# Performance work log

Hardware: AMD Instinct MI355X
Metric: run time of the kernel (lower is better)

Reference implementation:

```python
import jax, jax.numpy as jnp
import numpy as np

B, S, D = 4, 2048, 512
H = 8
DK = D // H
F = 2048  # filter_size
K = 9     # kernel_size
PAD = (K - 1) // 2
EPS = 1e-5


def layer_norm(x, gamma, beta):
    mu = jnp.mean(x, axis=-1, keepdims=True)
    var = jnp.var(x, axis=-1, keepdims=True)
    return (x - mu) * jax.lax.rsqrt(var + EPS) * gamma + beta


def conv1d(x_bcs, w_oik, b):
    # x: (B, C, S), w: (O, I, K) torch Conv1d layout, SAME padding
    y = jax.lax.conv_general_dilated(
        x_bcs, w_oik, window_strides=(1,), padding=[(PAD, PAD)],
        dimension_numbers=("NCH", "OIH", "NCH"))
    return y + b[None, :, None]


def setup_inputs() -> dict:
    key = jax.random.key(0)
    ks = jax.random.split(key, 16)
    g = lambda k, shp: (jax.random.normal(k, shp, dtype=jnp.float32) * 0.02)
    return {
        "src": jax.random.normal(ks[0], (B, S, D), dtype=jnp.float32),
        "src_mask": jnp.ones((B, 1, S), dtype=bool),
        "wq": g(ks[1], (D, D)), "bq": jnp.zeros((D,), jnp.float32),
        "wk": g(ks[2], (D, D)), "bk": jnp.zeros((D,), jnp.float32),
        "wv": g(ks[3], (D, D)), "bv": jnp.zeros((D,), jnp.float32),
        "wo": g(ks[4], (D, D)), "bo": jnp.zeros((D,), jnp.float32),
        "conv1_w": g(ks[5], (F, D, K)), "conv1_b": jnp.zeros((F,), jnp.float32),
        "conv2_w": g(ks[6], (D, F, K)), "conv2_b": jnp.zeros((D,), jnp.float32),
        "g1": jnp.ones((D,), jnp.float32), "b1": jnp.zeros((D,), jnp.float32),
        "g2": jnp.ones((D,), jnp.float32), "b2": jnp.zeros((D,), jnp.float32),
    }


def reference(src, src_mask, wq, bq, wk, bk, wv, bv, wo, bo,
              conv1_w, conv1_b, conv2_w, conv2_b, g1, b1, g2, b2):
    # ---- multi-head self attention (naive, explicit score matrix) ----
    q = (src @ wq.T + bq).reshape(B, S, H, DK).transpose(0, 2, 1, 3)  # (B,H,S,DK)
    k = (src @ wk.T + bk).reshape(B, S, H, DK).transpose(0, 2, 1, 3)
    v = (src @ wv.T + bv).reshape(B, S, H, DK).transpose(0, 2, 1, 3)
    scores = jnp.einsum("bhqd,bhkd->bhqk", q, k) / jnp.sqrt(jnp.float32(DK))
    mask4 = src_mask[:, None, :, :]  # (B,1,1,S) broadcast over heads/queries
    scores = jnp.where(mask4, scores, jnp.float32(-1e9))
    attn = jax.nn.softmax(scores, axis=-1)
    ctx = jnp.einsum("bhqk,bhkd->bhqd", attn, v)
    ctx = ctx.transpose(0, 2, 1, 3).reshape(B, S, D)
    attn_out = ctx @ wo.T + bo
    x = layer_norm(src + attn_out, g1, b1)
    # ---- conv1d FFN ----
    h = x.transpose(0, 2, 1)                       # (B, D, S)
    h = jax.nn.relu(conv1d(h, conv1_w, conv1_b))   # (B, F, S)
    h = conv1d(h, conv2_w, conv2_b)                # (B, D, S)
    ffn_out = h.transpose(0, 2, 1)
    return layer_norm(x + ffn_out, g2, b2)
```

## Files before the change

kernel.cpp:

```cpp
#include <hip/hip_runtime.h>


#define DEV __device__ __forceinline__

typedef __attribute__((ext_vector_type(8))) short bf16x8_t;
typedef __attribute__((ext_vector_type(4))) float f32x4_t;

DEV unsigned short f2bf(float f) {
  union { float f; unsigned u; } c; c.f = f;
  return (unsigned short)((c.u + 0x7fffu + ((c.u >> 16) & 1u)) >> 16);
}
DEV float bf2f(unsigned short h) {
  union { unsigned u; float f; } c; c.u = ((unsigned)h) << 16;
  return c.f;
}

DEV void stage16(const unsigned short* g, unsigned short* lds_base, int lane) {
#if __has_builtin(__builtin_amdgcn_global_load_lds)
  (void)lane;
  __builtin_amdgcn_global_load_lds(
      (const __attribute__((address_space(1))) void*)g,
      (__attribute__((address_space(3))) void*)lds_base, 16, 0, 0);
#else
  *(bf16x8_t*)(lds_base + lane * 8) = *(const bf16x8_t*)g;
#endif
}

template <int CK, int OUTMODE, int N, int K, int LDA, int LDO, int KSPLIT>
__global__ __launch_bounds__(256, 4) void gemm_bt(
    const unsigned short* __restrict__ A, const unsigned short* __restrict__ B,
    const float* __restrict__ bias, void* __restrict__ out, void* __restrict__ out2,
    long pstride) {
  __shared__ __align__(16) unsigned short As[2][128 * 32];
  __shared__ __align__(16) unsigned short Bs[2][128 * 32];
  const int tid = threadIdx.x;
  const int lane = tid & 63, wave = tid >> 6;
  const int quad = lane >> 4, l16 = lane & 15;
  const int bm = blockIdx.x << 7, bn = blockIdx.y << 7;
  const int wr = (wave >> 1) << 6, wc = (wave & 1) << 6;
  const int k0 = blockIdx.z * KSPLIT;

  f32x4_t acc[4][4];
#pragma unroll
  for (int i = 0; i < 4; i++)
#pragma unroll
    for (int j = 0; j < 4; j++) acc[i][j] = (f32x4_t){0.f, 0.f, 0.f, 0.f};

  const int srow = (wave << 4) + (lane >> 2);
  const int scol = (lane & 3) << 3;

#pragma unroll 1
  for (int kb = 0; kb < KSPLIT; kb += 64) {
    __syncthreads();
#pragma unroll
    for (int h = 0; h < 2; h++) {
      const int k = k0 + kb + (h << 5);
      int ktap, kcol;
      if (CK > 0) { ktap = k / CK; kcol = k % CK; } else { ktap = 0; kcol = k; }
#pragma unroll
      for (int i = 0; i < 2; i++) {
        const int r = (i << 6) + srow;
        const int am = bm + r;
        const int arow = (CK > 0) ? (am + ((am >> 11) << 3) + ktap) : am;
        stage16(A + (long)arow * LDA + kcol + scol, &As[h][(i << 11) + (wave << 9)], lane);
        stage16(B + (long)(bn + r) * K + k + scol, &Bs[h][(i << 11) + (wave << 9)], lane);
      }
    }
    __syncthreads();

#pragma unroll
    for (int h = 0; h < 2; h++) {
      bf16x8_t af[4], bfr[4];
#pragma unroll
      for (int t = 0; t < 4; t++)
        af[t] = *(const bf16x8_t*)&As[h][((wr + (t << 4) + l16) << 5) + (quad << 3)];
#pragma unroll
      for (int t = 0; t < 4; t++)
        bfr[t] = *(const bf16x8_t*)&Bs[h][((wc + (t << 4) + l16) << 5) + (quad << 3)];
#pragma unroll
      for (int mt = 0; mt < 4; mt++)
#pragma unroll
        for (int nt = 0; nt < 4; nt++)
          acc[mt][nt] = __builtin_amdgcn_mfma_f32_16x16x32_bf16(af[mt], bfr[nt],
                                                                acc[mt][nt], 0, 0, 0);
    }
  }

  if (OUTMODE == 4) {
    const bool isqk = (blockIdx.y < 8);
#pragma unroll
    for (int mt = 0; mt < 4; mt++)
#pragma unroll
      for (int nt = 0; nt < 4; nt++) {
        const int col = bn + wc + (nt << 4) + l16;
        const float bv = bias[col];
        const int rowb = bm + wr + (mt << 4) + (quad << 2);
        if (isqk) {
#pragma unroll
          for (int r = 0; r < 4; r++)
            ((unsigned short*)out)[(long)(rowb + r) * 1024 + col] =
                f2bf(acc[mt][nt][r] + bv);
        } else {
          ushort4 pk;
          pk.x = f2bf(acc[mt][nt][0] + bv);
          pk.y = f2bf(acc[mt][nt][1] + bv);
          pk.z = f2bf(acc[mt][nt][2] + bv);
          pk.w = f2bf(acc[mt][nt][3] + bv);
          const int vcol = col - 1024;
          const int bb = rowb >> 11, s = rowb & 2047;
          *(ushort4*)((unsigned short*)out2 + ((long)(bb * 512 + vcol) << 11) + s) = pk;
        }
      }
    return;
  }

  unsigned short* po = (unsigned short*)out;
  if (OUTMODE == 3)
    po = (blockIdx.z == 3) ? (unsigned short*)out2
                           : (unsigned short*)out + (long)blockIdx.z * pstride;
  float* fo = (float*)out;
  if (OUTMODE == 1) fo = (blockIdx.z == 0) ? (float*)out : (float*)out2;

#pragma unroll
  for (int mt = 0; mt < 4; mt++)
#pragma unroll
    for (int nt = 0; nt < 4; nt++) {
      const int col = bn + wc + (nt << 4) + l16;
      float bv = 0.f;
      if (OUTMODE == 0 || OUTMODE == 2) bv = bias[col];
      if (OUTMODE == 1) bv = (blockIdx.z == 0) ? bias[col] : 0.f;
#pragma unroll
      for (int r = 0; r < 4; r++) {
        const int row = bm + wr + (mt << 4) + (quad << 2) + r;
        float v = acc[mt][nt][r] + bv;
        if (OUTMODE == 0) {
          ((unsigned short*)out)[(long)row * LDO + col] = f2bf(v);
        } else if (OUTMODE == 1) {
          fo[(long)row * LDO + col] = v;
        } else if (OUTMODE == 2) {
          v = v > 0.f ? v : 0.f;
          const int orow = row + ((row >> 11) << 3) + 4;
          ((unsigned short*)out)[(long)orow * LDO + col] = f2bf(v);
        } else {
          po[(long)row * LDO + col] = f2bf(v);
        }
      }
    }
}

__global__ __launch_bounds__(256) void flash_attn(
    const unsigned short* __restrict__ qk16, const unsigned short* __restrict__ vT,
    unsigned short* __restrict__ ctx16) {
  __shared__ __align__(16) unsigned short Ks[64 * 64];
  __shared__ __align__(16) unsigned short Vt[64 * 64];
  __shared__ __align__(16) unsigned short Ps[4][2][16 * 80];

  const int tid = threadIdx.x;
  const int lane = tid & 63, wave = tid >> 6;
  const int quad = lane >> 4, l16 = lane & 15;
  const int qt = blockIdx.x, bh = blockIdx.y;
  const int b = bh >> 3, h = bh & 7;
  const long rowbase = (long)b << 11;
  const int hoff = h << 6;
  const int qbase = (qt << 7) + (wave << 5);

  bf16x8_t qa[2][2];
#pragma unroll
  for (int hh = 0; hh < 2; hh++) {
    const long qrow = rowbase + qbase + (hh << 4) + l16;
    qa[hh][0] = *(const bf16x8_t*)(qk16 + (qrow << 10) + hoff + (quad << 3));
    qa[hh][1] = *(const bf16x8_t*)(qk16 + (qrow << 10) + hoff + 32 + (quad << 3));
  }
  bf16x8_t ones;
#pragma unroll
  for (int i = 0; i < 8; i++) ones[i] = (short)0x3F80;

  f32x4_t o[2][4];
#pragma unroll
  for (int hh = 0; hh < 2; hh++)
#pragma unroll
    for (int i = 0; i < 4; i++) o[hh][i] = (f32x4_t){0.f, 0.f, 0.f, 0.f};
  f32x4_t l4[2] = {{0.f, 0.f, 0.f, 0.f}, {0.f, 0.f, 0.f, 0.f}};

  const int srow8 = lane >> 3;
  const int scol8 = (lane & 7) << 3;
  const unsigned short* kbase = qk16 + 512;
  const unsigned short* vbase = vT + ((long)(b * 512 + hoff) << 11);

  for (int kt = 0; kt < 2048; kt += 64) {
    __syncthreads();
#pragma unroll
    for (int j = 0; j < 2; j++) {
      const int kr = (wave << 4) + (j << 3);
      stage16(kbase + ((rowbase + kt + kr + srow8) << 10) + hoff + scol8,
              &Ks[kr << 6], lane);
      stage16(vbase + ((long)(kr + srow8) << 11) + kt + scol8, &Vt[kr << 6], lane);
    }
    __syncthreads();

    bf16x8_t kf[4][2];
#pragma unroll
    for (int t = 0; t < 4; t++) {
      kf[t][0] = *(const bf16x8_t*)&Ks[(((t << 4) + l16) << 6) + (quad << 3)];
      kf[t][1] = *(const bf16x8_t*)&Ks[(((t << 4) + l16) << 6) + 32 + (quad << 3)];
    }
#pragma unroll
    for (int hh = 0; hh < 2; hh++) {
      f32x4_t s[4];
#pragma unroll
      for (int t = 0; t < 4; t++) s[t] = (f32x4_t){0.f, 0.f, 0.f, 0.f};
#pragma unroll
      for (int t = 0; t < 4; t++) {
        s[t] = __builtin_amdgcn_mfma_f32_16x16x32_bf16(qa[hh][0], kf[t][0], s[t], 0, 0, 0);
        s[t] = __builtin_amdgcn_mfma_f32_16x16x32_bf16(qa[hh][1], kf[t][1], s[t], 0, 0, 0);
      }
#pragma unroll
      for (int r = 0; r < 4; r++)
#pragma unroll
        for (int t = 0; t < 4; t++) {
          union { float f; unsigned u; } cv;
          cv.f = __expf(s[t][r] * 0.125f);
          Ps[wave][hh][((quad << 2) + r) * 80 + (t << 4) + l16] =
              (unsigned short)(cv.u >> 16);
        }
    }
    bf16x8_t vf[4][2];
#pragma unroll
    for (int t = 0; t < 4; t++) {
      vf[t][0] = *(const bf16x8_t*)&Vt[(((t << 4) + l16) << 6) + (quad << 3)];
      vf[t][1] = *(const bf16x8_t*)&Vt[(((t << 4) + l16) << 6) + 32 + (quad << 3)];
    }
#pragma unroll
    for (int hh = 0; hh < 2; hh++) {
      const bf16x8_t pa0 = *(const bf16x8_t*)&Ps[wave][hh][l16 * 80 + (quad << 3)];
      const bf16x8_t pa1 = *(const bf16x8_t*)&Ps[wave][hh][l16 * 80 + 32 + (quad << 3)];
      l4[hh] = __builtin_amdgcn_mfma_f32_16x16x32_bf16(pa0, ones, l4[hh], 0, 0, 0);
      l4[hh] = __builtin_amdgcn_mfma_f32_16x16x32_bf16(pa1, ones, l4[hh], 0, 0, 0);
#pragma unroll
      for (int dt = 0; dt < 4; dt++) {
        o[hh][dt] = __builtin_amdgcn_mfma_f32_16x16x32_bf16(pa0, vf[dt][0], o[hh][dt], 0, 0, 0);
        o[hh][dt] = __builtin_amdgcn_mfma_f32_16x16x32_bf16(pa1, vf[dt][1], o[hh][dt], 0, 0, 0);
      }
    }
  }

#pragma unroll
  for (int hh = 0; hh < 2; hh++)
#pragma unroll
    for (int r = 0; r < 4; r++) {
      const float inv = 1.f / l4[hh][r];
      const long orow = rowbase + qbase + (hh << 4) + (quad << 2) + r;
#pragma unroll
      for (int dt = 0; dt < 4; dt++)
        ctx16[(orow << 9) + hoff + (dt << 4) + l16] = f2bf(o[hh][dt][r] * inv);
    }
}

__global__ __launch_bounds__(256) void ln_fused(
    const float* __restrict__ xa, const float* __restrict__ xb,
    const float* __restrict__ xc, const float* __restrict__ gamma,
    const float* __restrict__ beta, unsigned short* __restrict__ padout) {
  const int lane = threadIdx.x & 63, wave = threadIdx.x >> 6;
  const long row = ((long)blockIdx.x << 2) + wave;
  const long base = (row << 9) + (lane << 3);
  float s[8];
  {
    const float4 a0 = *(const float4*)(xa + base);
    const float4 a1 = *(const float4*)(xa + base + 4);
    const float4 b0 = *(const float4*)(xb + base);
    const float4 b1 = *(const float4*)(xb + base + 4);
    const float4 c0 = *(const float4*)(xc + base);
    const float4 c1 = *(const float4*)(xc + base + 4);
    s[0] = a0.x + b0.x + c0.x; s[1] = a0.y + b0.y + c0.y;
    s[2] = a0.z + b0.z + c0.z; s[3] = a0.w + b0.w + c0.w;
    s[4] = a1.x + b1.x + c1.x; s[5] = a1.y + b1.y + c1.y;
    s[6] = a1.z + b1.z + c1.z; s[7] = a1.w + b1.w + c1.w;
  }
  float sum = 0.f, sq = 0.f;
#pragma unroll
  for (int i = 0; i < 8; i++) { sum += s[i]; sq += s[i] * s[i]; }
#pragma unroll
  for (int d = 1; d < 64; d <<= 1) { sum += __shfl_xor(sum, d); sq += __shfl_xor(sq, d); }
  const float mean = sum * (1.f / 512.f);
  const float var = sq * (1.f / 512.f) - mean * mean;
  const float rstd = rsqrtf(var + 1e-5f);
  const int col = lane << 3;
  const long prow = row + ((row >> 11) << 3) + 4;
  bf16x8_t pv;
#pragma unroll
  for (int i = 0; i < 8; i++)
    pv[i] = (short)f2bf((s[i] - mean) * rstd * gamma[col + i] + beta[col + i]);
  *(bf16x8_t*)(padout + (prow << 9) + (lane << 3)) = pv;
}

__global__ __launch_bounds__(256) void ln2_red(
    const unsigned short* __restrict__ xpad, const unsigned short* __restrict__ pA,
    const unsigned short* __restrict__ pB, const float* __restrict__ bias,
    const float* __restrict__ gamma, const float* __restrict__ beta,
    float* __restrict__ out) {
  const int lane = threadIdx.x & 63, wave = threadIdx.x >> 6;
  const long row = ((long)blockIdx.x << 2) + wave;
  const long base = (row << 9) + (lane << 3);
  const int col = lane << 3;
  const long prow = row + ((row >> 11) << 3) + 4;
  const bf16x8_t xr = *(const bf16x8_t*)(xpad + (prow << 9) + (lane << 3));
  const bf16x8_t p0 = *(const bf16x8_t*)(pA + base);
  const bf16x8_t p1 = *(const bf16x8_t*)(pA + 4194304 + base);
  const bf16x8_t p2 = *(const bf16x8_t*)(pA + 8388608 + base);
  const bf16x8_t p3 = *(const bf16x8_t*)(pB + base);
  float s[8];
#pragma unroll
  for (int i = 0; i < 8; i++) {
    s[i] = bf2f((unsigned short)xr[i]) + bias[col + i] +
           bf2f((unsigned short)p0[i]) + bf2f((unsigned short)p1[i]) +
           bf2f((unsigned short)p2[i]) + bf2f((unsigned short)p3[i]);
  }
  float sum = 0.f, sq = 0.f;
#pragma unroll
  for (int i = 0; i < 8; i++) { sum += s[i]; sq += s[i] * s[i]; }
#pragma unroll
  for (int d = 1; d < 64; d <<= 1) { sum += __shfl_xor(sum, d); sq += __shfl_xor(sq, d); }
  const float mean = sum * (1.f / 512.f);
  const float var = sq * (1.f / 512.f) - mean * mean;
  const float rstd = rsqrtf(var + 1e-5f);
  float y[8];
#pragma unroll
  for (int i = 0; i < 8; i++) y[i] = (s[i] - mean) * rstd * gamma[col + i] + beta[col + i];
  float4 y0 = {y[0], y[1], y[2], y[3]}, y1 = {y[4], y[5], y[6], y[7]};
  *(float4*)(out + base) = y0;
  *(float4*)(out + base + 4) = y1;
}

__global__ void prep(const float* __restrict__ src, unsigned short* __restrict__ src16,
                     const float* __restrict__ wq, const float* __restrict__ wk,
                     const float* __restrict__ wv, const float* __restrict__ wo,
                     unsigned short* __restrict__ wqkv16, unsigned short* __restrict__ wo16,
                     const float* __restrict__ c1w, unsigned short* __restrict__ w1p,
                     const float* __restrict__ c2w, unsigned short* __restrict__ w2p,
                     unsigned short* __restrict__ xpad,
                     const float* __restrict__ bq, const float* __restrict__ bk,
                     const float* __restrict__ bv, float* __restrict__ bqkv) {
  const int bid = blockIdx.x, tid = threadIdx.x;
  if (bid < 4096) {
    const int i = bid * 256 + tid;
    const float4 v = ((const float4*)src)[i];
    ushort4 r; r.x = f2bf(v.x); r.y = f2bf(v.y); r.z = f2bf(v.z); r.w = f2bf(v.w);
    ((ushort4*)src16)[i] = r;
  } else if (bid < 5120) {
    const int w = (bid - 4096) >> 8;
    const int i = ((bid - 4096) & 255) * 256 + tid;
    const float* sp = (w == 0) ? wq : (w == 1) ? wk : (w == 2) ? wv : wo;
    unsigned short* dp = (w < 3) ? (wqkv16 + (w << 18)) : wo16;
    const float4 v = ((const float4*)sp)[i];
    ushort4 r; r.x = f2bf(v.x); r.y = f2bf(v.y); r.z = f2bf(v.z); r.w = f2bf(v.w);
    ((ushort4*)dp)[i] = r;
  } else if (bid < 9216) {
    const int idx = (bid - 5120) * 256 + tid;
    const int c = idx & 511, f = idx >> 9;
    float vals[9];
#pragma unroll
    for (int k = 0; k < 9; k++) vals[k] = c1w[(long)idx * 9 + k];
#pragma unroll
    for (int k = 0; k < 9; k++)
      w1p[(((long)f * 9 + k) << 9) + c] = f2bf(vals[k]);
  } else if (bid < 13312) {
    const int idx = (bid - 9216) * 256 + tid;
    const int c = idx & 2047, f = idx >> 11;
    float vals[9];
#pragma unroll
    for (int k = 0; k < 9; k++) vals[k] = c2w[(long)idx * 9 + k];
#pragma unroll
    for (int k = 0; k < 9; k++)
      w2p[(((long)f * 9 + k) << 11) + c] = f2bf(vals[k]);
  } else if (bid < 13376) {
    const int i = (bid - 13312) * 256 + tid;
    const int b = i >> 12, r = (i >> 9) & 7, c = i & 511;
    const int t = (r < 4) ? r : 2048 + r;
    xpad[((long)b * 2056 + t) * 512 + c] = 0;
  } else {
    const int i = (bid - 13376) * 256 + tid;
    bqkv[i] = (i < 512) ? bq[i] : (i < 1024) ? bk[i - 512] : bv[i - 1024];
  }
}

__global__ void zero_hpad(unsigned short* __restrict__ hpad) {
  const long j = (long)blockIdx.x * 256 + threadIdx.x;
  const int b = j >> 14, r = (j >> 11) & 7, c = j & 2047;
  const int t = (r < 4) ? r : 2048 + r;
  hpad[((long)b * 2056 + t) * 2048 + c] = 0;
}

extern "C" void kernel_launch(void* const* d_in, const int* in_sizes, int n_in,
                              void* d_out, int out_size, void* d_ws, size_t ws_size,
                              hipStream_t stream) {
  (void)in_sizes; (void)n_in; (void)out_size; (void)ws_size;
  const float* src = (const float*)d_in[0];
  const float* wq = (const float*)d_in[2];  const float* bq = (const float*)d_in[3];
  const float* wk = (const float*)d_in[4];  const float* bk = (const float*)d_in[5];
  const float* wv = (const float*)d_in[6];  const float* bv = (const float*)d_in[7];
  const float* wo = (const float*)d_in[8];  const float* bo = (const float*)d_in[9];
  const float* c1w = (const float*)d_in[10]; const float* c1b = (const float*)d_in[11];
  const float* c2w = (const float*)d_in[12]; const float* c2b = (const float*)d_in[13];
  const float* g1 = (const float*)d_in[14]; const float* b1 = (const float*)d_in[15];
  const float* g2 = (const float*)d_in[16]; const float* b2 = (const float*)d_in[17];
  float* out = (float*)d_out;

  char* ws = (char*)d_ws;
  unsigned short* src16  = (unsigned short*)(ws + 0);
  unsigned short* wqkv16 = (unsigned short*)(ws + 8388608);
  unsigned short* wo16   = wqkv16 + 786432;
  unsigned short* qk16   = (unsigned short*)(ws + 10485760);
  float* proj1           = (float*)(ws + 10485760);
  unsigned short* vT     = (unsigned short*)(ws + 27262976);
  unsigned short* ctx16  = (unsigned short*)(ws + 35651584);
  float* bqkv            = (float*)(ws + 35651584);
  float* attn_out        = (float*)(ws + 44040192);
  unsigned short* xpad   = (unsigned short*)(ws + 77594624);
  unsigned short* w1p    = (unsigned short*)(ws + 86016000);
  unsigned short* w2p    = (unsigned short*)(ws + 104890368);
  unsigned short* hpad   = (unsigned short*)(ws + 0);
  unsigned short* pA     = (unsigned short*)(ws + 35651584);
  unsigned short* pB     = (unsigned short*)(ws + 60817408);

  prep<<<13382, 256, 0, stream>>>(src, src16, wq, wk, wv, wo, wqkv16, wo16,
                                  c1w, w1p, c2w, w2p, xpad, bq, bk, bv, bqkv);

  gemm_bt<0, 4, 1536, 512, 512, 1024, 512><<<dim3(64, 12, 1), 256, 0, stream>>>(
      src16, wqkv16, bqkv, qk16, vT, 0);

  flash_attn<<<dim3(16, 32), 256, 0, stream>>>(qk16, vT, ctx16);

  gemm_bt<0, 1, 512, 512, 512, 512, 256><<<dim3(64, 4, 2), 256, 0, stream>>>(
      ctx16, wo16, bo, attn_out, proj1, 0);

  ln_fused<<<2048, 256, 0, stream>>>(src, attn_out, proj1, g1, b1, xpad);

  zero_hpad<<<256, 256, 0, stream>>>(hpad);

  gemm_bt<512, 2, 2048, 4608, 512, 2048, 4608><<<dim3(64, 16, 1), 256, 0, stream>>>(
      xpad, w1p, c1b, hpad, nullptr, 0);

  gemm_bt<2048, 3, 512, 18432, 2048, 512, 4608><<<dim3(64, 4, 4), 256, 0, stream>>>(
      hpad, w2p, nullptr, pA, pB, 4194304);

  ln2_red<<<2048, 256, 0, stream>>>(xpad, pA, pB, c2b, g2, b2, out);
}
```

Before: 620.9 us.

## Add 256x256-tile 8-wave pipelined GEMM for the two conv FFN layers

Adds a new GEMM kernel with 512 threads and 256x256 output tiles. It double-buffers A and B in LDS, loads through global_load_lds with XOR swizzling, and interleaves the next tile's loads with the MFMA phases, using explicit waitcnt, barriers and setprio. The two convolution GEMMs, conv1 with ReLU and padded output and conv2 with split-K partials, now use it in place of the 128-tile gemm_bt. The goal is more data reuse per block and better overlap of memory with MFMA. The cost is fewer blocks (256 for conv1 and conv2 each), higher register and LDS pressure, and fragile manual scheduling.

```diff
diff --git a/kernel.cpp b/kernel.cpp
--- a/kernel.cpp
+++ b/kernel.cpp
@@ -141,6 +141,145 @@
           v = v > 0.f ? v : 0.f;
           const int orow = row + ((row >> 11) << 3) + 4;
           ((unsigned short*)out)[(long)orow * LDO + col] = f2bf(v);
+        } else {
+          po[(long)row * LDO + col] = f2bf(v);
+        }
+      }
+    }
+}
+
+template <int CK, int OUTMODE, int KB, int LDA, int LDO, int KSPLIT>
+__global__ __launch_bounds__(512, 2) void gemm8p(
+    const unsigned short* __restrict__ A, const unsigned short* __restrict__ B,
+    const float* __restrict__ bias, void* __restrict__ out,
+    void* __restrict__ out2, long pstride) {
+  __shared__ __align__(16) unsigned short lds[2][4][128 * 64];
+  constexpr int NT = KSPLIT / 64;
+  const int tid = threadIdx.x;
+  const int lane = tid & 63, wave = tid >> 6;
+  const int quad = lane >> 4, l16 = lane & 15;
+  const int wm = wave >> 2, wn = wave & 3;
+  const int bm = blockIdx.x << 8, bn = blockIdx.y << 8;
+  const int k0 = blockIdx.z * KSPLIT;
+  const int srow = lane >> 3;
+  const int scol = ((lane & 7) ^ srow) << 3;
+  const int pad8 = (bm >> 11) << 3;
+  const int fc = (quad << 3) ^ ((l16 & 7) << 3);
+  const int brow0 = (wn & 1) << 6;
+
+  f32x4_t acc[8][4];
+#pragma unroll
+  for (int i = 0; i < 8; i++)
+#pragma unroll
+    for (int j = 0; j < 4; j++) acc[i][j] = (f32x4_t){0.f, 0.f, 0.f, 0.f};
+
+  auto stageA = [&](int buf, int u, int h) {
+    const int kk = k0 + (u << 6);
+    int ktap = 0, kcb = kk;
+    if (CK > 0) { ktap = kk / CK; kcb = kk % CK; }
+#pragma unroll
+    for (int i = 0; i < 2; i++) {
+      const int rb = ((wave << 1) + i) << 3;
+      const int am = bm + (h << 7) + rb + srow;
+      const int arow = (CK > 0) ? (am + pad8 + ktap) : am;
+      stage16(A + (long)arow * LDA + kcb + scol, &lds[buf][h][rb << 6], lane);
+    }
+  };
+  auto stageB = [&](int buf, int u, int h) {
+    const int kk = k0 + (u << 6);
+#pragma unroll
+    for (int i = 0; i < 2; i++) {
+      const int rb = ((wave << 1) + i) << 3;
+      stage16(B + (long)(bn + (h << 7) + rb + srow) * KB + kk + scol,
+              &lds[buf][2 + h][rb << 6], lane);
+    }
+  };
+
+  stageA(0, 0, 0); stageA(0, 0, 1); stageB(0, 0, 0); stageB(0, 0, 1);
+  if (NT > 1) {
+    stageB(1, 1, 0); stageB(1, 1, 1);
+    asm volatile("s_waitcnt vmcnt(4)" ::: "memory");
+  } else {
+    asm volatile("s_waitcnt vmcnt(0)" ::: "memory");
+  }
+  __builtin_amdgcn_s_barrier();
+  __builtin_amdgcn_sched_barrier(0);
+
+#pragma unroll 1
+  for (int u = 0; u < NT; ++u) {
+    const int buf = u & 1;
+    const unsigned short* Ah = &lds[buf][wm][0];
+    const unsigned short* Bh = &lds[buf][2 + (wn >> 1)][0];
+    bf16x8_t bfr[4][2];
+#pragma unroll
+    for (int qd = 0; qd < 4; qd++) {
+      bf16x8_t af[2][2];
+#pragma unroll
+      for (int j = 0; j < 2; j++)
+#pragma unroll
+        for (int ks = 0; ks < 2; ks++) {
+          const int row = (((qd << 1) + j) << 4) + l16;
+          af[j][ks] = *(const bf16x8_t*)&Ah[(row << 6) + (fc ^ (ks << 5))];
+        }
+      if (qd == 0) {
+#pragma unroll
+        for (int nt = 0; nt < 4; nt++)
+#pragma unroll
+          for (int ks = 0; ks < 2; ks++) {
+            const int row = brow0 + (nt << 4) + l16;
+            bfr[nt][ks] = *(const bf16x8_t*)&Bh[(row << 6) + (fc ^ (ks << 5))];
+          }
+      }
+      if (qd == 0 && u + 1 < NT) stageA(buf ^ 1, u + 1, 0);
+      if (qd == 1 && u + 1 < NT) stageA(buf ^ 1, u + 1, 1);
+      if (qd == 2 && u + 2 < NT) stageB(buf, u + 2, 0);
+      if (qd == 3 && u + 2 < NT) stageB(buf, u + 2, 1);
+
+      __builtin_amdgcn_sched_barrier(0);
+      __builtin_amdgcn_s_barrier();
+      asm volatile("s_waitcnt lgkmcnt(0)" ::: "memory");
+      __builtin_amdgcn_sched_barrier(0);
+      __builtin_amdgcn_s_setprio(1);
+#pragma unroll
+      for (int ks = 0; ks < 2; ks++)
+#pragma unroll
+        for (int j = 0; j < 2; j++)
+#pragma unroll
+          for (int nt = 0; nt < 4; nt++)
+            acc[(qd << 1) + j][nt] = __builtin_amdgcn_mfma_f32_16x16x32_bf16(
+                af[j][ks], bfr[nt][ks], acc[(qd << 1) + j][nt], 0, 0, 0);
+      __builtin_amdgcn_s_setprio(0);
+      __builtin_amdgcn_sched_barrier(0);
+      if (qd < 3) {
+        __builtin_amdgcn_s_barrier();
+      } else if (u + 1 < NT) {
+        if (u + 2 < NT) asm volatile("s_waitcnt vmcnt(4)" ::: "memory");
+        else            asm volatile("s_waitcnt vmcnt(0)" ::: "memory");
+        __builtin_amdgcn_s_barrier();
+        __builtin_amdgcn_sched_barrier(0);
+      }
+    }
+  }
+
+  unsigned short* po = (unsigned short*)out;
+  if (OUTMODE == 3)
+    po = (blockIdx.z == 3) ? (unsigned short*)out2
+                           : (unsigned short*)out + (long)blockIdx.z * pstride;
+#pragma unroll
+  for (int mt = 0; mt < 8; mt++)
+#pragma unroll
+    for (int nt = 0; nt < 4; nt++) {
+      const int col = bn + (wn << 6) + (nt << 4) + l16;
+      float bv = 0.f;
+      if (OUTMODE == 2) bv = bias[col];
+#pragma unroll
+      for (int r = 0; r < 4; r++) {
+        const int row = bm + (wm << 7) + (mt << 4) + (quad << 2) + r;
+        float v = acc[mt][nt][r] + bv;
+        if (OUTMODE == 2) {
+          v = v > 0.f ? v : 0.f;
+          const int orow = row + ((row >> 11) << 3) + 4;
+          po[(long)orow * LDO + col] = f2bf(v);
         } else {
           po[(long)row * LDO + col] = f2bf(v);
         }
@@ -437,10 +576,10 @@
 
   zero_hpad<<<256, 256, 0, stream>>>(hpad);
 
-  gemm_bt<512, 2, 2048, 4608, 512, 2048, 4608><<<dim3(64, 16, 1), 256, 0, stream>>>(
+  gemm8p<512, 2, 4608, 512, 2048, 4608><<<dim3(32, 8, 1), 512, 0, stream>>>(
       xpad, w1p, c1b, hpad, nullptr, 0);
 
-  gemm_bt<2048, 3, 512, 18432, 2048, 512, 4608><<<dim3(64, 4, 4), 256, 0, stream>>>(
+  gemm8p<2048, 3, 18432, 2048, 512, 4608><<<dim3(32, 2, 4), 512, 0, stream>>>(
       hpad, w2p, nullptr, pA, pB, 4194304);
 
   ln2_red<<<2048, 256, 0, stream>>>(xpad, pA, pB, c2b, g2, b2, out);
```

After: 545.4 us. -12.2%, faster.
